# Kernel optimization log

Measured on AMD Instinct MI355X. Metric: run time of the kernel, lower is better.

Reference implementation:

```python
import jax, jax.numpy as jnp
import numpy as np

MASS = 0.5
G = 1.0  # constant offset -p[8]*g in the objective; does not affect argmin u*
NEWTON_ITERS = 30


def _lambertw(x):
    """Solve w*exp(w) = x for x >= 0 (principal branch) via Newton iterations."""
    w = jnp.log1p(x)  # good init on [0, inf)
    for _ in range(NEWTON_ITERS):
        ew = jnp.exp(w)
        w = w - (w * ew - x) / (ew * (w + 1.0))
    return w


def setup_inputs() -> dict:
    key = jax.random.key(0)
    kz, kt, k1, k2 = jax.random.split(key, 4)
    B, S, H = 500000, 12, 100
    return {
        "z": jax.random.normal(kz, (B, S), jnp.float32),
        "t": jax.random.uniform(kt, (B,), jnp.float32),
        "W1": jax.random.normal(k1, (S + 1, H), jnp.float32) * 0.1,
        "b1": jnp.zeros((H,), jnp.float32),
        "W2": jax.random.normal(k2, (H, S), jnp.float32) * 0.1,
        "b2": jnp.zeros((S,), jnp.float32),
    }


def reference(z, t, W1, b1, W2, b2):
    # p_net: MLP on concat([t, z])
    inp = jnp.concatenate([t[:, None], z], axis=1)          # [B, 13]
    h = jnp.tanh(inp @ W1 + b1)                              # [B, 100]
    p = h @ W2 + b2                                          # [B, 12]
    # Objective: c . u + exp(0.5*||u||^2) + const, with
    # c = [(p6+p7+p8)/m, p9, p10, p11]. Stationarity: c + u*exp(0.5||u||^2)=0
    # => u = -c*exp(-0.5*w), where w = ||u||^2 solves w*e^w = ||c||^2 (Lambert W).
    c = jnp.stack(
        [(p[:, 6] + p[:, 7] + p[:, 8]) / MASS, p[:, 9], p[:, 10], p[:, 11]],
        axis=1,
    )                                                        # [B, 4]
    x = jnp.sum(c * c, axis=1)                               # [B] = ||c||^2
    w = _lambertw(x)                                         # [B]
    ustar = -c * jnp.exp(-0.5 * w)[:, None]                  # [B, 4]
    return ustar
```

## Files before the change

### kernel.cpp

```cpp
#include <hip/hip_runtime.h>


constexpr int S = 12;
constexpr int H = 100;

__device__ __forceinline__ float fast_rcp(float x) {
    return __builtin_amdgcn_rcpf(x);
}

__device__ __forceinline__ float fast_tanh(float x) {
    float e = __expf(2.0f * x);
    return fmaf(-2.0f, fast_rcp(1.0f + e), 1.0f);
}

__global__ __launch_bounds__(256) void cvx_quad_kernel(
    const float* __restrict__ z, const float* __restrict__ t,
    const float* __restrict__ W1, const float* __restrict__ b1,
    const float* __restrict__ W2, const float* __restrict__ b2,
    float* __restrict__ out, int B)
{
    int tid = blockIdx.x * 256 + threadIdx.x;
    int i0 = tid * 2;
    if (i0 >= B) return;

    float inpA[S + 1], inpB[S + 1];
    inpA[0] = t[i0];
    inpB[0] = t[i0 + 1];
    const float4* zr = reinterpret_cast<const float4*>(z) + (size_t)i0 * 3;
    float4 a0 = zr[0], a1 = zr[1], a2 = zr[2];
    float4 c0v = zr[3], c1v = zr[4], c2v = zr[5];
    inpA[1]  = a0.x; inpA[2]  = a0.y; inpA[3]  = a0.z; inpA[4]  = a0.w;
    inpA[5]  = a1.x; inpA[6]  = a1.y; inpA[7]  = a1.z; inpA[8]  = a1.w;
    inpA[9]  = a2.x; inpA[10] = a2.y; inpA[11] = a2.z; inpA[12] = a2.w;
    inpB[1]  = c0v.x; inpB[2]  = c0v.y; inpB[3]  = c0v.z; inpB[4]  = c0v.w;
    inpB[5]  = c1v.x; inpB[6]  = c1v.y; inpB[7]  = c1v.z; inpB[8]  = c1v.w;
    inpB[9]  = c2v.x; inpB[10] = c2v.y; inpB[11] = c2v.z; inpB[12] = c2v.w;

    float pA[6], pB[6];
    #pragma unroll
    for (int m = 0; m < 6; ++m) {
        float bm = b2[6 + m];
        pA[m] = bm;
        pB[m] = bm;
    }

    #pragma unroll 2
    for (int j = 0; j < H; ++j) {
        float accA = b1[j];
        float accB = accA;
        const float* w1c = W1 + j;
        #pragma unroll
        for (int k = 0; k < S + 1; ++k) {
            float w = w1c[k * H];
            accA = fmaf(inpA[k], w, accA);
            accB = fmaf(inpB[k], w, accB);
        }
        float thA = fast_tanh(accA);
        float thB = fast_tanh(accB);
        const float* w2r = W2 + j * S + 6;
        #pragma unroll
        for (int m = 0; m < 6; ++m) {
            float w = w2r[m];
            pA[m] = fmaf(thA, w, pA[m]);
            pB[m] = fmaf(thB, w, pB[m]);
        }
    }

    #pragma unroll
    for (int e = 0; e < 2; ++e) {
        const float* p = e ? pB : pA;
        float c0 = 2.0f * (p[0] + p[1] + p[2]);
        float c1 = p[3], c2 = p[4], c3 = p[5];
        float x = fmaf(c0, c0, fmaf(c1, c1, fmaf(c2, c2, c3 * c3)));

        float w = __logf(1.0f + x);
        #pragma unroll
        for (int it = 0; it < 6; ++it) {
            float ew  = __expf(w);
            float num = fmaf(w, ew, -x);
            float den = fmaf(ew, w, ew);
            w = w - num * fast_rcp(den);
        }

        float sc = -__expf(-0.5f * w);
        float4 o;
        o.x = c0 * sc;
        o.y = c1 * sc;
        o.z = c2 * sc;
        o.w = c3 * sc;
        reinterpret_cast<float4*>(out)[i0 + e] = o;
    }
}

extern "C" void kernel_launch(void* const* d_in, const int* in_sizes, int n_in,
                              void* d_out, int out_size, void* d_ws, size_t ws_size,
                              hipStream_t stream) {
    const float* z  = (const float*)d_in[0];
    const float* t  = (const float*)d_in[1];
    const float* W1 = (const float*)d_in[2];
    const float* b1 = (const float*)d_in[3];
    const float* W2 = (const float*)d_in[4];
    const float* b2 = (const float*)d_in[5];
    float* out = (float*)d_out;

    int B = in_sizes[1];
    int threads = (B + 1) / 2;
    int grid = (threads + 255) / 256;
    cvx_quad_kernel<<<dim3(grid), dim3(256), 0, stream>>>(z, t, W1, b1, W2, b2, out, B);
}
```

Baseline: 116.0 us.

## Use packed fp16 dot products for MLP layers with prepacked weights

A small pre-kernel packs W1 (pre-scaled by 2*log2e), b1 and W2 into fp16 pairs in workspace. The main kernel then runs both MLP layers with v_dot2 fp16 instructions, two hidden units per step. tanh uses exp2, and one shared reciprocal covers each pair of units. The Newton iterations drop from 6 to 5. This halves the FMA count, but fp16 rounding of inputs, weights and activations adds error, and there is an extra kernel launch.

```diff
diff --git a/kernel.cpp b/kernel.cpp
--- a/kernel.cpp
+++ b/kernel.cpp
@@ -3,38 +3,111 @@
 
 constexpr int S = 12;
 constexpr int H = 100;
+#define TWO_LOG2E 2.8853900817779268f
+
+typedef _Float16 h2 __attribute__((ext_vector_type(2)));
 
 __device__ __forceinline__ float fast_rcp(float x) {
     return __builtin_amdgcn_rcpf(x);
 }
 
-__device__ __forceinline__ float fast_tanh(float x) {
-    float e = __expf(2.0f * x);
-    return fmaf(-2.0f, fast_rcp(1.0f + e), 1.0f);
+__device__ __forceinline__ h2 bit_h2(unsigned int u) {
+    union { unsigned int u; h2 h; } cv; cv.u = u; return cv.h;
+}
+
+#if __has_builtin(__builtin_amdgcn_fdot2)
+__device__ __forceinline__ float fdot2(h2 a, h2 b, float c) {
+    return __builtin_amdgcn_fdot2(a, b, c, false);
+}
+#else
+__device__ __forceinline__ float fdot2(h2 a, h2 b, float c) {
+    return fmaf((float)a.x, (float)b.x, fmaf((float)a.y, (float)b.y, c));
+}
+#endif
+
+__device__ __forceinline__ h2 pk16(float a, float b) {
+#if __has_builtin(__builtin_amdgcn_cvt_pkrtz)
+    union {
+        __fp16 __attribute__((ext_vector_type(2))) f;
+        h2 h;
+    } cv;
+    cv.f = __builtin_amdgcn_cvt_pkrtz(a, b);
+    return cv.h;
+#else
+    h2 r; r.x = (_Float16)a; r.y = (_Float16)b; return r;
+#endif
+}
+
+__global__ __launch_bounds__(256) void pack_weights(
+    const float* __restrict__ W1, const float* __restrict__ b1,
+    const float* __restrict__ W2, unsigned int* __restrict__ ws)
+{
+    int idx = blockIdx.x * 256 + threadIdx.x;
+    if (idx < 800) {
+        int jp = idx >> 4, s = idx & 15;
+        unsigned int v;
+        if (s < 14) {
+            int unit = 2 * jp + (s >= 7);
+            int q = (s < 7) ? s : s - 7;
+            int k0 = 2 * q, k1 = 2 * q + 1;
+            float w0 = W1[k0 * H + unit] * TWO_LOG2E;
+            float w1 = (k1 < 13) ? W1[k1 * H + unit] * TWO_LOG2E : 0.0f;
+            union { h2 h; unsigned int u; } cv;
+            cv.h = pk16(w0, w1);
+            v = cv.u;
+        } else {
+            int unit = 2 * jp + (s - 14);
+            union { float f; unsigned int u; } cv;
+            cv.f = b1[unit] * TWO_LOG2E;
+            v = cv.u;
+        }
+        ws[idx] = v;
+    } else if (idx < 1200) {
+        int r = idx - 800;
+        int jp = r >> 3, m = r & 7;
+        unsigned int v = 0;
+        if (m < 6) {
+            float w0 = W2[(2 * jp) * S + 6 + m];
+            float w1 = W2[(2 * jp + 1) * S + 6 + m];
+            union { h2 h; unsigned int u; } cv;
+            cv.h = pk16(w0, w1);
+            v = cv.u;
+        }
+        ws[idx] = v;
+    }
 }
 
 __global__ __launch_bounds__(256) void cvx_quad_kernel(
     const float* __restrict__ z, const float* __restrict__ t,
-    const float* __restrict__ W1, const float* __restrict__ b1,
-    const float* __restrict__ W2, const float* __restrict__ b2,
+    const unsigned int* __restrict__ ws, const float* __restrict__ b2,
     float* __restrict__ out, int B)
 {
     int tid = blockIdx.x * 256 + threadIdx.x;
     int i0 = tid * 2;
     if (i0 >= B) return;
-
-    float inpA[S + 1], inpB[S + 1];
-    inpA[0] = t[i0];
-    inpB[0] = t[i0 + 1];
-    const float4* zr = reinterpret_cast<const float4*>(z) + (size_t)i0 * 3;
-    float4 a0 = zr[0], a1 = zr[1], a2 = zr[2];
-    float4 c0v = zr[3], c1v = zr[4], c2v = zr[5];
-    inpA[1]  = a0.x; inpA[2]  = a0.y; inpA[3]  = a0.z; inpA[4]  = a0.w;
-    inpA[5]  = a1.x; inpA[6]  = a1.y; inpA[7]  = a1.z; inpA[8]  = a1.w;
-    inpA[9]  = a2.x; inpA[10] = a2.y; inpA[11] = a2.z; inpA[12] = a2.w;
-    inpB[1]  = c0v.x; inpB[2]  = c0v.y; inpB[3]  = c0v.z; inpB[4]  = c0v.w;
-    inpB[5]  = c1v.x; inpB[6]  = c1v.y; inpB[7]  = c1v.z; inpB[8]  = c1v.w;
-    inpB[9]  = c2v.x; inpB[10] = c2v.y; inpB[11] = c2v.z; inpB[12] = c2v.w;
+    int i1 = (i0 + 1 < B) ? (i0 + 1) : (B - 1);
+
+    h2 inA[7], inB[7];
+    {
+        const float4* zr0 = reinterpret_cast<const float4*>(z) + (size_t)i0 * 3;
+        const float4* zr1 = reinterpret_cast<const float4*>(z) + (size_t)i1 * 3;
+        float4 a0 = zr0[0], a1 = zr0[1], a2 = zr0[2];
+        float4 d0 = zr1[0], d1 = zr1[1], d2 = zr1[2];
+        inA[0] = pk16(t[i0], a0.x);
+        inA[1] = pk16(a0.y, a0.z);
+        inA[2] = pk16(a0.w, a1.x);
+        inA[3] = pk16(a1.y, a1.z);
+        inA[4] = pk16(a1.w, a2.x);
+        inA[5] = pk16(a2.y, a2.z);
+        inA[6] = pk16(a2.w, 0.0f);
+        inB[0] = pk16(t[i1], d0.x);
+        inB[1] = pk16(d0.y, d0.z);
+        inB[2] = pk16(d0.w, d1.x);
+        inB[3] = pk16(d1.y, d1.z);
+        inB[4] = pk16(d1.w, d2.x);
+        inB[5] = pk16(d2.y, d2.z);
+        inB[6] = pk16(d2.w, 0.0f);
+    }
 
     float pA[6], pB[6];
     #pragma unroll
@@ -45,24 +118,41 @@
     }
 
     #pragma unroll 2
-    for (int j = 0; j < H; ++j) {
-        float accA = b1[j];
-        float accB = accA;
-        const float* w1c = W1 + j;
+    for (int jp = 0; jp < H / 2; ++jp) {
+        const unsigned int* ra = ws + jp * 16;
+        const unsigned int* rb = ws + 800 + jp * 8;
+
+        float fb0 = __uint_as_float(ra[14]);
+        float fb1 = __uint_as_float(ra[15]);
+        float accA0 = fb0, accA1 = fb1, accB0 = fb0, accB1 = fb1;
         #pragma unroll
-        for (int k = 0; k < S + 1; ++k) {
-            float w = w1c[k * H];
-            accA = fmaf(inpA[k], w, accA);
-            accB = fmaf(inpB[k], w, accB);
-        }
-        float thA = fast_tanh(accA);
-        float thB = fast_tanh(accB);
-        const float* w2r = W2 + j * S + 6;
+        for (int q = 0; q < 7; ++q) {
+            h2 w0 = bit_h2(ra[q]);
+            h2 w1 = bit_h2(ra[7 + q]);
+            accA0 = fdot2(inA[q], w0, accA0);
+            accA1 = fdot2(inA[q], w1, accA1);
+            accB0 = fdot2(inB[q], w0, accB0);
+            accB1 = fdot2(inB[q], w1, accB1);
+        }
+
+        float aA0 = 1.0f + __builtin_amdgcn_exp2f(accA0);
+        float aA1 = 1.0f + __builtin_amdgcn_exp2f(accA1);
+        float aB0 = 1.0f + __builtin_amdgcn_exp2f(accB0);
+        float aB1 = 1.0f + __builtin_amdgcn_exp2f(accB1);
+        float sA = -2.0f * fast_rcp(aA0 * aA1);
+        float sB = -2.0f * fast_rcp(aB0 * aB1);
+        float thA0 = fmaf(aA1, sA, 1.0f);
+        float thA1 = fmaf(aA0, sA, 1.0f);
+        float thB0 = fmaf(aB1, sB, 1.0f);
+        float thB1 = fmaf(aB0, sB, 1.0f);
+        h2 tA = pk16(thA0, thA1);
+        h2 tB = pk16(thB0, thB1);
+
         #pragma unroll
         for (int m = 0; m < 6; ++m) {
-            float w = w2r[m];
-            pA[m] = fmaf(thA, w, pA[m]);
-            pB[m] = fmaf(thB, w, pB[m]);
+            h2 qm = bit_h2(rb[m]);
+            pA[m] = fdot2(tA, qm, pA[m]);
+            pB[m] = fdot2(tB, qm, pB[m]);
         }
     }
 
@@ -75,7 +165,7 @@
 
         float w = __logf(1.0f + x);
         #pragma unroll
-        for (int it = 0; it < 6; ++it) {
+        for (int it = 0; it < 5; ++it) {
             float ew  = __expf(w);
             float num = fmaf(w, ew, -x);
             float den = fmaf(ew, w, ew);
@@ -88,7 +178,7 @@
         o.y = c1 * sc;
         o.z = c2 * sc;
         o.w = c3 * sc;
-        reinterpret_cast<float4*>(out)[i0 + e] = o;
+        reinterpret_cast<float4*>(out)[e ? i1 : i0] = o;
     }
 }
 
@@ -102,9 +192,12 @@
     const float* W2 = (const float*)d_in[4];
     const float* b2 = (const float*)d_in[5];
     float* out = (float*)d_out;
+    unsigned int* ws = (unsigned int*)d_ws;
+
+    pack_weights<<<dim3(5), dim3(256), 0, stream>>>(W1, b1, W2, ws);
 
     int B = in_sizes[1];
     int threads = (B + 1) / 2;
     int grid = (threads + 255) / 256;
-    cvx_quad_kernel<<<dim3(grid), dim3(256), 0, stream>>>(z, t, W1, b1, W2, b2, out, B);
-}
+    cvx_quad_kernel<<<dim3(grid), dim3(256), 0, stream>>>(z, t, ws, b2, out, B);
+}
```

After: 104.8 us. 9.7% less time.
